# Optimization experiments

Hardware: AMD Instinct MI355X
Metric: run time of the kernel (lower is better)

Reference implementation:

```python
import jax, jax.numpy as jnp
import numpy as np
from jax import lax

SEQ_LEN = 1024
BATCH = 256
INPUT_SIZE = 64
STATE_SIZE = 960
STREAM_SIZE = INPUT_SIZE + STATE_SIZE  # 1024
OUTPUT_SIZE = 64
IDENTITY_PROPORTION = 0.97


def _xavier_uniform(key, shape):
    fan_in, fan_out = shape[1], shape[0]
    limit = np.sqrt(6.0 / (fan_in + fan_out)).astype(np.float32)
    return jax.random.uniform(key, shape, jnp.float32, -limit, limit)


def setup_inputs() -> dict:
    key = jax.random.key(0)
    k_x, k_w1, k_w2 = jax.random.split(key, 3)
    return {
        "input": jax.random.normal(k_x, (SEQ_LEN, BATCH, INPUT_SIZE), jnp.float32),
        "W1": _xavier_uniform(k_w1, (STREAM_SIZE, STREAM_SIZE)),
        "b1": jnp.zeros((STREAM_SIZE,), jnp.float32),
        "W2": _xavier_uniform(k_w2, (STREAM_SIZE, STREAM_SIZE)),
        "b2": jnp.zeros((STREAM_SIZE,), jnp.float32),
    }


def reference(input, W1, b1, W2, b2):
    p = jnp.asarray(IDENTITY_PROPORTION, input.dtype)

    def step(stream, x_t):
        # Shift: prepend new input, trim to stream width.
        # stream: (B, STREAM_SIZE), x_t: (B, INPUT_SIZE)
        s = jnp.concatenate([x_t, stream], axis=-1)[..., :STREAM_SIZE]
        # Res block: abs nonlinearity + residual mix.
        h = jnp.abs(s @ W1.T + b1)
        s = p * s + (1.0 - p) * (h @ W2.T + b2)
        return s, None

    init = jnp.zeros((input.shape[1], STREAM_SIZE), input.dtype)
    final_stream, _ = lax.scan(step, init, input)
    return final_stream[..., -OUTPUT_SIZE:]
```

## Files before the change

### kernel.cpp

```cpp
#include <hip/hip_runtime.h>
#include <hip/hip_bf16.h>
#include <stdint.h>


#define NSTEP  1024
#define BATCH  256
#define INSZ   64
#define SSZ    1024

#define GROUPS 8
#define CBLKS  32
#define RPG    32
#define CPB    32
#define FPAD   16

typedef __bf16 bf16x8 __attribute__((ext_vector_type(8)));
typedef float  f32x4  __attribute__((ext_vector_type(4)));

#define SCHED_FENCE() __builtin_amdgcn_sched_barrier(0)
#define WAITV8() do { asm volatile("s_waitcnt vmcnt(8)" ::: "memory"); SCHED_FENCE(); } while (0)
#define WAITV0() do { asm volatile("s_waitcnt vmcnt(0)" ::: "memory"); SCHED_FENCE(); } while (0)

__device__ __forceinline__ void issue8(const char* p,
    bf16x8& r0, bf16x8& r1, bf16x8& r2, bf16x8& r3,
    bf16x8& r4, bf16x8& r5, bf16x8& r6, bf16x8& r7)
{
    asm volatile(
        "global_load_dwordx4 %0, %8, off sc0 sc1\n\t"
        "global_load_dwordx4 %1, %8, off offset:64 sc0 sc1\n\t"
        "global_load_dwordx4 %2, %8, off offset:128 sc0 sc1\n\t"
        "global_load_dwordx4 %3, %8, off offset:192 sc0 sc1\n\t"
        "global_load_dwordx4 %4, %8, off offset:256 sc0 sc1\n\t"
        "global_load_dwordx4 %5, %8, off offset:320 sc0 sc1\n\t"
        "global_load_dwordx4 %6, %8, off offset:384 sc0 sc1\n\t"
        "global_load_dwordx4 %7, %8, off offset:448 sc0 sc1"
        : "=&v"(r0), "=&v"(r1), "=&v"(r2), "=&v"(r3),
          "=&v"(r4), "=&v"(r5), "=&v"(r6), "=&v"(r7)
        : "v"(p) : "memory");
}

__device__ __forceinline__ void issue4f(const float* p0, const float* p1,
                                        const float* p2, const float* p3,
                                        float& r0, float& r1, float& r2, float& r3)
{
    asm volatile(
        "global_load_dword %0, %4, off sc0 sc1\n\t"
        "global_load_dword %1, %5, off sc0 sc1\n\t"
        "global_load_dword %2, %6, off sc0 sc1\n\t"
        "global_load_dword %3, %7, off sc0 sc1"
        : "=&v"(r0), "=&v"(r1), "=&v"(r2), "=&v"(r3)
        : "v"(p0), "v"(p1), "v"(p2), "v"(p3)
        : "memory");
}

__device__ __forceinline__ void st_coh_u16(void* p, unsigned short v) {
    asm volatile("global_store_short %0, %1, off sc0 sc1" :: "v"(p), "v"(v) : "memory");
}
__device__ __forceinline__ void st_coh_f32(void* p, float v) {
    asm volatile("global_store_dword %0, %1, off sc0 sc1" :: "v"(p), "v"(v) : "memory");
}

__device__ __forceinline__ void group_barrier(unsigned* flags, int g, int c,
                                              unsigned e, int tid)
{
    asm volatile("s_waitcnt vmcnt(0)" ::: "memory");
    __syncthreads();
    if (tid == 0)
        __hip_atomic_store(&flags[(g * CBLKS + c) * FPAD], e, __ATOMIC_RELAXED,
                           __HIP_MEMORY_SCOPE_AGENT);
    if (tid < 64) {
        uint64_t t0 = __builtin_amdgcn_s_memrealtime();
        for (;;) {
            unsigned v = e;
            if (tid < CBLKS)
                v = __hip_atomic_load(&flags[(g * CBLKS + tid) * FPAD], __ATOMIC_RELAXED,
                                      __HIP_MEMORY_SCOPE_AGENT);
            if (!__any((int)(v - e) < 0)) break;
            if (__builtin_amdgcn_s_memrealtime() - t0 > 400000ull) break;
        }
    }
    __syncthreads();
}

#define MFMA8(BASE, A0, A1, A2, A3, A4, A5, A6, A7)                                        \
    do {                                                                                   \
        acc0 = __builtin_amdgcn_mfma_f32_16x16x32_bf16(A0,                                 \
            *reinterpret_cast<const bf16x8*>(Bw + ((((BASE) + 0) * 64 + kbyte) ^ bswz)),   \
            acc0, 0, 0, 0);                                                                \
        acc1 = __builtin_amdgcn_mfma_f32_16x16x32_bf16(A1,                                 \
            *reinterpret_cast<const bf16x8*>(Bw + ((((BASE) + 1) * 64 + kbyte) ^ bswz)),   \
            acc1, 0, 0, 0);                                                                \
        acc2 = __builtin_amdgcn_mfma_f32_16x16x32_bf16(A2,                                 \
            *reinterpret_cast<const bf16x8*>(Bw + ((((BASE) + 2) * 64 + kbyte) ^ bswz)),   \
            acc2, 0, 0, 0);                                                                \
        acc3 = __builtin_amdgcn_mfma_f32_16x16x32_bf16(A3,                                 \
            *reinterpret_cast<const bf16x8*>(Bw + ((((BASE) + 3) * 64 + kbyte) ^ bswz)),   \
            acc3, 0, 0, 0);                                                                \
        acc0 = __builtin_amdgcn_mfma_f32_16x16x32_bf16(A4,                                 \
            *reinterpret_cast<const bf16x8*>(Bw + ((((BASE) + 4) * 64 + kbyte) ^ bswz)),   \
            acc0, 0, 0, 0);                                                                \
        acc1 = __builtin_amdgcn_mfma_f32_16x16x32_bf16(A5,                                 \
            *reinterpret_cast<const bf16x8*>(Bw + ((((BASE) + 5) * 64 + kbyte) ^ bswz)),   \
            acc1, 0, 0, 0);                                                                \
        acc2 = __builtin_amdgcn_mfma_f32_16x16x32_bf16(A6,                                 \
            *reinterpret_cast<const bf16x8*>(Bw + ((((BASE) + 6) * 64 + kbyte) ^ bswz)),   \
            acc2, 0, 0, 0);                                                                \
        acc3 = __builtin_amdgcn_mfma_f32_16x16x32_bf16(A7,                                 \
            *reinterpret_cast<const bf16x8*>(Bw + ((((BASE) + 7) * 64 + kbyte) ^ bswz)),   \
            acc3, 0, 0, 0);                                                                \
    } while (0)

__device__ __forceinline__ f32x4 phase_mm(const char* Ab, const char* Bw,
                                          int kbyte, int bswz)
{
    f32x4 acc0 = {0.f, 0.f, 0.f, 0.f}, acc1 = acc0, acc2 = acc0, acc3 = acc0;
    bf16x8 x0, x1, x2, x3, x4, x5, x6, x7;
    bf16x8 y0, y1, y2, y3, y4, y5, y6, y7;

    issue8(Ab,        x0, x1, x2, x3, x4, x5, x6, x7);
    issue8(Ab +  512, y0, y1, y2, y3, y4, y5, y6, y7);
    WAITV8();
    MFMA8(0,  x0, x1, x2, x3, x4, x5, x6, x7);
    issue8(Ab + 1024, x0, x1, x2, x3, x4, x5, x6, x7);
    WAITV8();
    MFMA8(8,  y0, y1, y2, y3, y4, y5, y6, y7);
    issue8(Ab + 1536, y0, y1, y2, y3, y4, y5, y6, y7);
    WAITV8();
    MFMA8(16, x0, x1, x2, x3, x4, x5, x6, x7);
    WAITV0();
    MFMA8(24, y0, y1, y2, y3, y4, y5, y6, y7);

    return (acc0 + acc1) + (acc2 + acc3);
}

extern "C" __global__ void __launch_bounds__(256, 1)
resrnn_kernel(const float* __restrict__ x,  const float* __restrict__ W1,
              const float* __restrict__ b1, const float* __restrict__ W2,
              const float* __restrict__ b2,
              __bf16* sBuf, __bf16* hBuf, float* sf32, unsigned* flags,
              float* __restrict__ dout)
{
    extern __shared__ char smem[];
    char* W1s = smem;
    char* W2s = smem + 65536;

    const int tid = threadIdx.x;
    const int bid = blockIdx.x;
    const int g   = bid & 7;
    const int c   = bid >> 3;
    const int rb  = g * RPG;
    const int cb  = c * CPB;

    {
        const int lc  = tid >> 3;
        const int seg = (tid & 7) * 128;
        const int sw  = (lc & 7) << 4;
        const float* w1p = W1 + (size_t)(cb + lc) * SSZ + seg;
        const float* w2p = W2 + (size_t)(cb + lc) * SSZ + seg;
        char* d1 = W1s + lc * 2048;
        char* d2 = W2s + lc * 2048;
        #pragma unroll 4
        for (int kk = 0; kk < 16; ++kk) {
            const int kb = (seg + kk * 8) * 2;
            float4 f0 = reinterpret_cast<const float4*>(w1p)[kk * 2 + 0];
            float4 f1 = reinterpret_cast<const float4*>(w1p)[kk * 2 + 1];
            bf16x8 v;
            v[0] = (__bf16)f0.x; v[1] = (__bf16)f0.y; v[2] = (__bf16)f0.z; v[3] = (__bf16)f0.w;
            v[4] = (__bf16)f1.x; v[5] = (__bf16)f1.y; v[6] = (__bf16)f1.z; v[7] = (__bf16)f1.w;
            *reinterpret_cast<bf16x8*>(d1 + (kb ^ sw)) = v;
            f0 = reinterpret_cast<const float4*>(w2p)[kk * 2 + 0];
            f1 = reinterpret_cast<const float4*>(w2p)[kk * 2 + 1];
            v[0] = (__bf16)f0.x; v[1] = (__bf16)f0.y; v[2] = (__bf16)f0.z; v[3] = (__bf16)f0.w;
            v[4] = (__bf16)f1.x; v[5] = (__bf16)f1.y; v[6] = (__bf16)f1.z; v[7] = (__bf16)f1.w;
            *reinterpret_cast<bf16x8*>(d2 + (kb ^ sw)) = v;
        }
    }

    {
        const int e0  = tid * 4;
        const int row = rb + (e0 >> 5);
        const int col = cb + (e0 & 31);
        float* sp32 = sf32 + (size_t)row * SSZ + col;
        st_coh_f32(sp32 + 0, 0.f); st_coh_f32(sp32 + 1, 0.f);
        st_coh_f32(sp32 + 2, 0.f); st_coh_f32(sp32 + 3, 0.f);
        __bf16* sp = sBuf + (size_t)row * SSZ + col;
        if (c < 2) {
            const float* xp = x + (size_t)row * INSZ + col;
            #pragma unroll
            for (int i = 0; i < 4; ++i)
                st_coh_u16(sp + i, __builtin_bit_cast(unsigned short, (__bf16)xp[i]));
        } else {
            #pragma unroll
            for (int i = 0; i < 4; ++i)
                st_coh_u16(sp + i, __builtin_bit_cast(unsigned short, (__bf16)0.f));
        }
    }

    group_barrier(flags, g, c, 1u, tid);

    const int lane  = tid & 63;
    const int wv    = tid >> 6;
    const int mh    = wv >> 1;
    const int nh    = wv & 1;
    const int kgrp  = lane >> 4;
    const int kbyte = kgrp * 16;
    const int arow  = rb + mh * 16 + (lane & 15);
    const char* AbS = (const char*)sBuf + (size_t)arow * 2048 + kgrp * 16;
    const char* AbH = (const char*)hBuf + (size_t)arow * 2048 + kgrp * 16;
    const int lc    = nh * 16 + (lane & 15);
    const int bswz  = (lc & 7) << 4;
    const char* Bw1 = W1s + lc * 2048;
    const char* Bw2 = W2s + lc * 2048;
    const float bias1 = b1[cb + lc];
    const float bias2 = b2[cb + lc];
    const int drow0 = rb + mh * 16 + kgrp * 4;
    const int dcol  = cb + lc;
    const float P = 0.97f, OMP = 1.0f - 0.97f;

    for (int t = 0; t < NSTEP; ++t) {
        {
            const char* Bw = Bw1;
            f32x4 h4 = phase_mm(AbS, Bw, kbyte, bswz);
            #pragma unroll
            for (int j = 0; j < 4; ++j) {
                float hv = fabsf(h4[j] + bias1);
                st_coh_u16(hBuf + (size_t)(drow0 + j) * SSZ + dcol,
                           __builtin_bit_cast(unsigned short, (__bf16)hv));
            }
        }

        const float* srd = sf32 + (size_t)(t & 1) * (BATCH * SSZ);
        float sp0, sp1, sp2, sp3;
        if (c < 2) {
            const float* xp = x + (size_t)t * (BATCH * INSZ);
            sp0 = xp[(size_t)(drow0 + 0) * INSZ + dcol];
            sp1 = xp[(size_t)(drow0 + 1) * INSZ + dcol];
            sp2 = xp[(size_t)(drow0 + 2) * INSZ + dcol];
            sp3 = xp[(size_t)(drow0 + 3) * INSZ + dcol];
        } else {
            issue4f(&srd[(size_t)(drow0 + 0) * SSZ + (dcol - 64)],
                    &srd[(size_t)(drow0 + 1) * SSZ + (dcol - 64)],
                    &srd[(size_t)(drow0 + 2) * SSZ + (dcol - 64)],
                    &srd[(size_t)(drow0 + 3) * SSZ + (dcol - 64)],
                    sp0, sp1, sp2, sp3);
        }

        group_barrier(flags, g, c, (unsigned)(2 + 2 * t), tid);

        f32x4 u4 = phase_mm(AbH, Bw2, kbyte, bswz);

        float*  swr = sf32 + (size_t)((t + 1) & 1) * (BATCH * SSZ);
        float spv[4] = {sp0, sp1, sp2, sp3};
        #pragma unroll
        for (int j = 0; j < 4; ++j) {
            const int row = drow0 + j;
            const float snew = P * spv[j] + OMP * (u4[j] + bias2);
            st_coh_f32(&swr[(size_t)row * SSZ + dcol], snew);
            if (c < 30)
                st_coh_u16(sBuf + (size_t)row * SSZ + (dcol + 64),
                           __builtin_bit_cast(unsigned short, (__bf16)snew));
            else if (t == NSTEP - 1)
                dout[row * 64 + (dcol - 960)] = snew;
        }
        if (c < 2 && t < NSTEP - 1) {
            #pragma unroll
            for (int j = 0; j < 4; ++j) {
                const int row = drow0 + j;
                st_coh_u16(sBuf + (size_t)row * SSZ + dcol,
                           __builtin_bit_cast(unsigned short,
                               (__bf16)x[(size_t)(t + 1) * (BATCH * INSZ) +
                                         (size_t)row * INSZ + dcol]));
            }
        }
        if (t < NSTEP - 1)
            group_barrier(flags, g, c, (unsigned)(3 + 2 * t), tid);
    }
}

extern "C" void kernel_launch(void* const* d_in, const int* in_sizes, int n_in,
                              void* d_out, int out_size, void* d_ws, size_t ws_size,
                              hipStream_t stream)
{
    const float* x  = (const float*)d_in[0];
    const float* W1 = (const float*)d_in[1];
    const float* b1 = (const float*)d_in[2];
    const float* W2 = (const float*)d_in[3];
    const float* b2 = (const float*)d_in[4];
    float* dout = (float*)d_out;

    char* ws = (char*)d_ws;
    __bf16*   sBuf  = (__bf16*)(ws);
    __bf16*   hBuf  = (__bf16*)(ws + (512 << 10));
    float*    sf32  = (float*)(ws + (1 << 20));
    unsigned* flags = (unsigned*)(ws + (3 << 20));

    (void)in_sizes; (void)n_in; (void)out_size; (void)ws_size;

    hipFuncSetAttribute(reinterpret_cast<const void*>(&resrnn_kernel),
                        hipFuncAttributeMaxDynamicSharedMemorySize, 131072);
    hipLaunchKernelGGL(resrnn_kernel, dim3(256), dim3(256), 131072, stream,
                       x, W1, b1, W2, b2, sBuf, hBuf, sf32, flags, dout);
}
```

Before: 11.41 ms.

## Stage outputs through LDS for vectorized coherent stores and issue all A loads upfront

Per-step h and s results are first written to an LDS transpose tile, then each thread emits vectorized dwordx2/dwordx4 coherent global stores instead of many scattered 2-byte and 4-byte stores. The matmul phase now issues all 32 A-operand loads before any MFMA and uses graded vmcnt waits, giving deeper memory-level parallelism. In exchange each phase gains an extra __syncthreads, register pressure rises, and shared memory grows past 128KB.

```diff
diff --git a/kernel.cpp b/kernel.cpp
--- a/kernel.cpp
+++ b/kernel.cpp
@@ -13,13 +13,14 @@
 #define RPG    32
 #define CPB    32
 #define FPAD   16
-
-typedef __bf16 bf16x8 __attribute__((ext_vector_type(8)));
-typedef float  f32x4  __attribute__((ext_vector_type(4)));
+#define TSTR   36
+
+typedef __bf16  bf16x8 __attribute__((ext_vector_type(8)));
+typedef float   f32x4  __attribute__((ext_vector_type(4)));
+typedef unsigned u32x2 __attribute__((ext_vector_type(2)));
 
 #define SCHED_FENCE() __builtin_amdgcn_sched_barrier(0)
-#define WAITV8() do { asm volatile("s_waitcnt vmcnt(8)" ::: "memory"); SCHED_FENCE(); } while (0)
-#define WAITV0() do { asm volatile("s_waitcnt vmcnt(0)" ::: "memory"); SCHED_FENCE(); } while (0)
+#define WAITN(n) do { asm volatile("s_waitcnt vmcnt(" #n ")" ::: "memory"); SCHED_FENCE(); } while (0)
 
 __device__ __forceinline__ void issue8(const char* p,
     bf16x8& r0, bf16x8& r1, bf16x8& r2, bf16x8& r3,
@@ -58,6 +59,21 @@
 }
 __device__ __forceinline__ void st_coh_f32(void* p, float v) {
     asm volatile("global_store_dword %0, %1, off sc0 sc1" :: "v"(p), "v"(v) : "memory");
+}
+__device__ __forceinline__ void st_coh_b64(void* p, u32x2 v) {
+    asm volatile("global_store_dwordx2 %0, %1, off sc0 sc1" :: "v"(p), "v"(v) : "memory");
+}
+__device__ __forceinline__ void st_coh_b128(void* p, f32x4 v) {
+    asm volatile("global_store_dwordx4 %0, %1, off sc0 sc1" :: "v"(p), "v"(v) : "memory");
+}
+
+__device__ __forceinline__ u32x2 pack_bf16x4(f32x4 f) {
+    unsigned a = __builtin_bit_cast(unsigned short, (__bf16)f[0]);
+    unsigned b = __builtin_bit_cast(unsigned short, (__bf16)f[1]);
+    unsigned c = __builtin_bit_cast(unsigned short, (__bf16)f[2]);
+    unsigned d = __builtin_bit_cast(unsigned short, (__bf16)f[3]);
+    u32x2 r; r[0] = a | (b << 16); r[1] = c | (d << 16);
+    return r;
 }
 
 __device__ __forceinline__ void group_barrier(unsigned* flags, int g, int c,
@@ -114,21 +130,19 @@
                                           int kbyte, int bswz)
 {
     f32x4 acc0 = {0.f, 0.f, 0.f, 0.f}, acc1 = acc0, acc2 = acc0, acc3 = acc0;
-    bf16x8 x0, x1, x2, x3, x4, x5, x6, x7;
-    bf16x8 y0, y1, y2, y3, y4, y5, y6, y7;
-
-    issue8(Ab,        x0, x1, x2, x3, x4, x5, x6, x7);
-    issue8(Ab +  512, y0, y1, y2, y3, y4, y5, y6, y7);
-    WAITV8();
-    MFMA8(0,  x0, x1, x2, x3, x4, x5, x6, x7);
-    issue8(Ab + 1024, x0, x1, x2, x3, x4, x5, x6, x7);
-    WAITV8();
-    MFMA8(8,  y0, y1, y2, y3, y4, y5, y6, y7);
-    issue8(Ab + 1536, y0, y1, y2, y3, y4, y5, y6, y7);
-    WAITV8();
-    MFMA8(16, x0, x1, x2, x3, x4, x5, x6, x7);
-    WAITV0();
-    MFMA8(24, y0, y1, y2, y3, y4, y5, y6, y7);
+    bf16x8 a0, a1, a2, a3, a4, a5, a6, a7;
+    bf16x8 b0, b1, b2, b3, b4, b5, b6, b7;
+    bf16x8 e0, e1, e2, e3, e4, e5, e6, e7;
+    bf16x8 d0, d1, d2, d3, d4, d5, d6, d7;
+
+    issue8(Ab,        a0, a1, a2, a3, a4, a5, a6, a7);
+    issue8(Ab +  512, b0, b1, b2, b3, b4, b5, b6, b7);
+    issue8(Ab + 1024, e0, e1, e2, e3, e4, e5, e6, e7);
+    issue8(Ab + 1536, d0, d1, d2, d3, d4, d5, d6, d7);
+    WAITN(24); MFMA8(0,  a0, a1, a2, a3, a4, a5, a6, a7);
+    WAITN(16); MFMA8(8,  b0, b1, b2, b3, b4, b5, b6, b7);
+    WAITN(8);  MFMA8(16, e0, e1, e2, e3, e4, e5, e6, e7);
+    WAITN(0);  MFMA8(24, d0, d1, d2, d3, d4, d5, d6, d7);
 
     return (acc0 + acc1) + (acc2 + acc3);
 }
@@ -141,8 +155,9 @@
               float* __restrict__ dout)
 {
     extern __shared__ char smem[];
-    char* W1s = smem;
-    char* W2s = smem + 65536;
+    char*  W1s = smem;
+    char*  W2s = smem + 65536;
+    float* T   = (float*)(smem + 131072);
 
     const int tid = threadIdx.x;
     const int bid = blockIdx.x;
@@ -152,26 +167,26 @@
     const int cb  = c * CPB;
 
     {
-        const int lc  = tid >> 3;
+        const int lcw = tid >> 3;
         const int seg = (tid & 7) * 128;
-        const int sw  = (lc & 7) << 4;
-        const float* w1p = W1 + (size_t)(cb + lc) * SSZ + seg;
-        const float* w2p = W2 + (size_t)(cb + lc) * SSZ + seg;
-        char* d1 = W1s + lc * 2048;
-        char* d2 = W2s + lc * 2048;
+        const int sw  = (lcw & 7) << 4;
+        const float* w1p = W1 + (size_t)(cb + lcw) * SSZ + seg;
+        const float* w2p = W2 + (size_t)(cb + lcw) * SSZ + seg;
+        char* d1 = W1s + lcw * 2048;
+        char* d2 = W2s + lcw * 2048;
         #pragma unroll 4
         for (int kk = 0; kk < 16; ++kk) {
             const int kb = (seg + kk * 8) * 2;
-            float4 f0 = reinterpret_cast<const float4*>(w1p)[kk * 2 + 0];
-            float4 f1 = reinterpret_cast<const float4*>(w1p)[kk * 2 + 1];
+            f32x4 f0 = reinterpret_cast<const f32x4*>(w1p)[kk * 2 + 0];
+            f32x4 f1 = reinterpret_cast<const f32x4*>(w1p)[kk * 2 + 1];
             bf16x8 v;
-            v[0] = (__bf16)f0.x; v[1] = (__bf16)f0.y; v[2] = (__bf16)f0.z; v[3] = (__bf16)f0.w;
-            v[4] = (__bf16)f1.x; v[5] = (__bf16)f1.y; v[6] = (__bf16)f1.z; v[7] = (__bf16)f1.w;
+            v[0] = (__bf16)f0[0]; v[1] = (__bf16)f0[1]; v[2] = (__bf16)f0[2]; v[3] = (__bf16)f0[3];
+            v[4] = (__bf16)f1[0]; v[5] = (__bf16)f1[1]; v[6] = (__bf16)f1[2]; v[7] = (__bf16)f1[3];
             *reinterpret_cast<bf16x8*>(d1 + (kb ^ sw)) = v;
-            f0 = reinterpret_cast<const float4*>(w2p)[kk * 2 + 0];
-            f1 = reinterpret_cast<const float4*>(w2p)[kk * 2 + 1];
-            v[0] = (__bf16)f0.x; v[1] = (__bf16)f0.y; v[2] = (__bf16)f0.z; v[3] = (__bf16)f0.w;
-            v[4] = (__bf16)f1.x; v[5] = (__bf16)f1.y; v[6] = (__bf16)f1.z; v[7] = (__bf16)f1.w;
+            f0 = reinterpret_cast<const f32x4*>(w2p)[kk * 2 + 0];
+            f1 = reinterpret_cast<const f32x4*>(w2p)[kk * 2 + 1];
+            v[0] = (__bf16)f0[0]; v[1] = (__bf16)f0[1]; v[2] = (__bf16)f0[2]; v[3] = (__bf16)f0[3];
+            v[4] = (__bf16)f1[0]; v[5] = (__bf16)f1[1]; v[6] = (__bf16)f1[2]; v[7] = (__bf16)f1[3];
             *reinterpret_cast<bf16x8*>(d2 + (kb ^ sw)) = v;
         }
     }
@@ -213,20 +228,25 @@
     const char* Bw2 = W2s + lc * 2048;
     const float bias1 = b1[cb + lc];
     const float bias2 = b2[cb + lc];
-    const int drow0 = rb + mh * 16 + kgrp * 4;
+    const int lrow0 = mh * 16 + kgrp * 4;
+    const int drow0 = rb + lrow0;
     const int dcol  = cb + lc;
     const float P = 0.97f, OMP = 1.0f - 0.97f;
 
+    const int srow = tid >> 3;
+    const int scol = (tid & 7) * 4;
+
     for (int t = 0; t < NSTEP; ++t) {
         {
-            const char* Bw = Bw1;
-            f32x4 h4 = phase_mm(AbS, Bw, kbyte, bswz);
+            f32x4 h4 = phase_mm(AbS, Bw1, kbyte, bswz);
             #pragma unroll
-            for (int j = 0; j < 4; ++j) {
-                float hv = fabsf(h4[j] + bias1);
-                st_coh_u16(hBuf + (size_t)(drow0 + j) * SSZ + dcol,
-                           __builtin_bit_cast(unsigned short, (__bf16)hv));
-            }
+            for (int j = 0; j < 4; ++j)
+                T[(lrow0 + j) * TSTR + lc] = fabsf(h4[j] + bias1);
+        }
+        __syncthreads();
+        {
+            f32x4 hv = *reinterpret_cast<const f32x4*>(&T[srow * TSTR + scol]);
+            st_coh_b64(hBuf + (size_t)(rb + srow) * SSZ + cb + scol, pack_bf16x4(hv));
         }
 
         const float* srd = sf32 + (size_t)(t & 1) * (BATCH * SSZ);
@@ -247,29 +267,28 @@
 
         group_barrier(flags, g, c, (unsigned)(2 + 2 * t), tid);
 
-        f32x4 u4 = phase_mm(AbH, Bw2, kbyte, bswz);
-
-        float*  swr = sf32 + (size_t)((t + 1) & 1) * (BATCH * SSZ);
-        float spv[4] = {sp0, sp1, sp2, sp3};
-        #pragma unroll
-        for (int j = 0; j < 4; ++j) {
-            const int row = drow0 + j;
-            const float snew = P * spv[j] + OMP * (u4[j] + bias2);
-            st_coh_f32(&swr[(size_t)row * SSZ + dcol], snew);
-            if (c < 30)
-                st_coh_u16(sBuf + (size_t)row * SSZ + (dcol + 64),
-                           __builtin_bit_cast(unsigned short, (__bf16)snew));
-            else if (t == NSTEP - 1)
-                dout[row * 64 + (dcol - 960)] = snew;
-        }
-        if (c < 2 && t < NSTEP - 1) {
+        {
+            f32x4 u4 = phase_mm(AbH, Bw2, kbyte, bswz);
+            const float spv[4] = {sp0, sp1, sp2, sp3};
             #pragma unroll
-            for (int j = 0; j < 4; ++j) {
-                const int row = drow0 + j;
-                st_coh_u16(sBuf + (size_t)row * SSZ + dcol,
-                           __builtin_bit_cast(unsigned short,
-                               (__bf16)x[(size_t)(t + 1) * (BATCH * INSZ) +
-                                         (size_t)row * INSZ + dcol]));
+            for (int j = 0; j < 4; ++j)
+                T[(lrow0 + j) * TSTR + lc] = P * spv[j] + OMP * (u4[j] + bias2);
+        }
+        __syncthreads();
+        {
+            float* swr = sf32 + (size_t)((t + 1) & 1) * (BATCH * SSZ);
+            f32x4 sv  = *reinterpret_cast<const f32x4*>(&T[srow * TSTR + scol]);
+            const int grow = rb + srow;
+            st_coh_b128(&swr[(size_t)grow * SSZ + cb + scol], sv);
+            if (c < 30) {
+                st_coh_b64(sBuf + (size_t)grow * SSZ + (cb + 64) + scol, pack_bf16x4(sv));
+            } else if (t == NSTEP - 1) {
+                *reinterpret_cast<f32x4*>(&dout[grow * 64 + (cb - 960) + scol]) = sv;
+            }
+            if (c < 2 && t < NSTEP - 1) {
+                f32x4 xv = *reinterpret_cast<const f32x4*>(
+                    &x[(size_t)(t + 1) * (BATCH * INSZ) + (size_t)grow * INSZ + cb + scol]);
+                st_coh_b64(sBuf + (size_t)grow * SSZ + cb + scol, pack_bf16x4(xv));
             }
         }
         if (t < NSTEP - 1)
@@ -296,8 +315,8 @@
 
     (void)in_sizes; (void)n_in; (void)out_size; (void)ws_size;
 
-    hipFuncSetAttribute(reinterpret_cast<const void*>(&resrnn_kernel),
-                        hipFuncAttributeMaxDynamicSharedMemorySize, 131072);
-    hipLaunchKernelGGL(resrnn_kernel, dim3(256), dim3(256), 131072, stream,
+    (void)hipFuncSetAttribute(reinterpret_cast<const void*>(&resrnn_kernel),
+                              hipFuncAttributeMaxDynamicSharedMemorySize, 135680);
+    hipLaunchKernelGGL(resrnn_kernel, dim3(256), dim3(256), 135680, stream,
                        x, W1, b1, W2, b2, sBuf, hBuf, sf32, flags, dout);
 }
```

New measurement: 10.90 ms. 1.05x faster.
